# Performance work log

Measured on AMD Instinct MI355X. Metric: run time of the kernel, lower is better.

Reference implementation:

```python
import jax, jax.numpy as jnp
import numpy as np

NUM_ENT = 10000
NUM_REL = 230
S_DIM = 96
T_DIM = 32
DIM = S_DIM + T_DIM  # 128
N = 32768   # neighbors
Q = 4096    # unique query entities
E = 32768   # pooling edges
B = 1024    # batch triples
BN_EPS = 1e-5


def setup_inputs() -> dict:
    key = jax.random.key(0)
    ks = jax.random.split(key, 32)
    inp = {}
    inp["neighbor_idx"] = jax.random.randint(ks[0], (N,), 0, NUM_ENT)
    inp["rel_id"] = jax.random.randint(ks[1], (N,), 0, 2 * NUM_REL)
    inp["years"] = jax.random.uniform(ks[2], (N, 1), jnp.float32)
    inp["months"] = jax.random.uniform(ks[3], (N, 1), jnp.float32)
    inp["days"] = jax.random.uniform(ks[4], (N, 1), jnp.float32)
    inp["pool_src"] = jax.random.randint(ks[5], (E,), 0, N)
    inp["pool_dst"] = jax.random.randint(ks[6], (E,), 0, Q)
    inp["head_pos"] = jax.random.randint(ks[7], (B,), 0, Q)
    inp["tail_pos"] = jax.random.randint(ks[8], (B,), 0, Q)
    inp["rels"] = jax.random.randint(ks[9], (B,), 0, NUM_REL)
    # parameters (xavier-ish scales)
    inp["ent_embs"] = jax.random.normal(ks[10], (NUM_ENT, S_DIM), jnp.float32) * 0.05
    names = ["y_freq", "y_phi", "y_amp", "m_freq", "m_phi", "m_amp", "d_freq", "d_phi", "d_amp"]
    for i, n in enumerate(names):
        inp[n] = jax.random.normal(ks[11 + i], (NUM_ENT, T_DIM), jnp.float32) * 0.05
    inp["rel_embs"] = jax.random.normal(ks[20], (NUM_REL, DIM), jnp.float32) * 0.05
    inp["W"] = jax.random.normal(ks[21], (2 * NUM_REL, DIM, DIM), jnp.float32) * (1.0 / np.sqrt(DIM))
    inp["b"] = jnp.zeros((2 * NUM_REL, DIM), jnp.float32)
    inp["gamma"] = jnp.ones((2 * NUM_REL, DIM), jnp.float32)
    inp["beta"] = jnp.zeros((2 * NUM_REL, DIM), jnp.float32)
    return inp


def _forward(ent_embs, y_freq, y_phi, y_amp, m_freq, m_phi, m_amp,
             d_freq, d_phi, d_amp, rel_embs, W, b, gamma, beta,
             years, months, days,
             neighbor_idx, rel_id, pool_src, pool_dst, head_pos, tail_pos, rels):
    # diachronic time embedding: amp * sin(freq * t + phi), summed over y/m/d
    ty = y_amp[neighbor_idx] * jnp.sin(y_freq[neighbor_idx] * years + y_phi[neighbor_idx])
    tm = m_amp[neighbor_idx] * jnp.sin(m_freq[neighbor_idx] * months + m_phi[neighbor_idx])
    td = d_amp[neighbor_idx] * jnp.sin(d_freq[neighbor_idx] * days + d_phi[neighbor_idx])
    x = jnp.concatenate([ent_embs[neighbor_idx], ty + tm + td], axis=1)  # [N, DIM]

    # per-relation Linear (gather weights per neighbor)
    z = jnp.einsum('nd,nde->ne', x, W[rel_id]) + b[rel_id]  # [N, DIM]

    # per-relation-bucket BatchNorm (training stats, biased var); skipped for singleton buckets
    R2 = 2 * NUM_REL
    cnt = jax.ops.segment_sum(jnp.ones((z.shape[0],), z.dtype), rel_id, num_segments=R2)
    denom = jnp.maximum(cnt, 1.0)[:, None]
    mean = jax.ops.segment_sum(z, rel_id, num_segments=R2) / denom
    var = jax.ops.segment_sum(z * z, rel_id, num_segments=R2) / denom - mean * mean
    var = jnp.maximum(var, 0.0)
    zn = (z - mean[rel_id]) * jax.lax.rsqrt(var[rel_id] + BN_EPS) * gamma[rel_id] + beta[rel_id]
    z = jnp.where((cnt[rel_id] > 1.0)[:, None], zn, z)
    z = jax.nn.relu(z)

    # average pooling of neighbor features per query entity (PoolingLayer 'avg')
    psum = jax.ops.segment_sum(z[pool_src], pool_dst, num_segments=Q)
    pcnt = jax.ops.segment_sum(jnp.ones((pool_src.shape[0],), z.dtype), pool_dst, num_segments=Q)
    emb = psum / jnp.maximum(pcnt, 1.0)[:, None]  # [Q, DIM]

    # TransE-style scoring: -||h + r - t||_2 (dropout p=0 / eval mode)
    diff = emb[head_pos] + rel_embs[rels] - emb[tail_pos]
    return -jnp.sqrt(jnp.sum(diff * diff, axis=1))


def reference(neighbor_idx, rel_id, years, months, days, pool_src, pool_dst,
              head_pos, tail_pos, rels, ent_embs, y_freq, y_phi, y_amp,
              m_freq, m_phi, m_amp, d_freq, d_phi, d_amp, rel_embs, W, b, gamma, beta):
    return _forward(ent_embs, y_freq, y_phi, y_amp, m_freq, m_phi, m_amp,
                    d_freq, d_phi, d_amp, rel_embs, W, b, gamma, beta,
                    years, months, days,
                    neighbor_idx, rel_id, pool_src, pool_dst, head_pos, tail_pos, rels)
```

## Files before the change

### kernel.cpp

```cpp
#include <hip/hip_runtime.h>
#include <math.h>

#define NUM_ENT 10000
#define NUM_REL 230
#define R2      460
#define S_DIM   96
#define T_DIM   32
#define DIM     128
#define N_NBR   32768
#define Q_ENT   4096
#define E_EDGE  32768
#define B_TRI   1024
#define BN_EPS  1e-5f
#define CHUNK   64

typedef __attribute__((ext_vector_type(8))) short bf16x8;
typedef __attribute__((ext_vector_type(4))) float f32x4;

__device__ __forceinline__ unsigned short f2bf(float f) {
    unsigned int u = __float_as_uint(f);
    u = (u + 0x7FFFu + ((u >> 16) & 1u)) >> 16;
    return (unsigned short)u;
}
__device__ __forceinline__ float bf2f(unsigned short us) {
    return __uint_as_float((unsigned int)us << 16);
}

__device__ __forceinline__ int XIDX(int m, int d) {
    return (m * DIM + d) ^ ((m & 7) << 3);
}

__global__ void k_zero(int* __restrict__ p, int n4) {
    int i = blockIdx.x * blockDim.x + threadIdx.x;
    if (i < n4) ((int4*)p)[i] = make_int4(0, 0, 0, 0);
}

__global__ __launch_bounds__(256, 2) void k_front(
    const float* __restrict__ W, unsigned short* __restrict__ Wfrag,
    const int* __restrict__ rel, const int* __restrict__ psrc,
    const int* __restrict__ pdst,
    int* __restrict__ hist_rel, int* __restrict__ histE,
    int* __restrict__ hist_dst,
    int* __restrict__ ticket_n, int* __restrict__ ticket_e,
    int* __restrict__ ticket_d)
{
    const int t = threadIdx.x;
    if (blockIdx.x >= R2) {
        const int i = (blockIdx.x - R2) * 256 + t;
        if (i < N_NBR) ticket_n[i] = atomicAdd(&hist_rel[rel[i]], 1);
        if (i < E_EDGE) {
            const int s = psrc[i];
            ticket_e[i] = atomicAdd(&histE[rel[s]], 1);
            ticket_d[i] = atomicAdd(&hist_dst[pdst[i]], 1);
        }
        return;
    }
    const int r = blockIdx.x;
    __shared__ float Wl[DIM * DIM];
    {
        const float4* Wg = (const float4*)(W + (size_t)r * DIM * DIM);
        float4* Wl4 = (float4*)Wl;
        #pragma unroll
        for (int i = 0; i < 16; ++i)
            Wl4[t + i * 256] = Wg[t + i * 256];
    }
    __syncthreads();
    unsigned short* dst = Wfrag + (size_t)r * DIM * DIM;
    #pragma unroll
    for (int it = 0; it < 8; ++it) {
        const int id = t + it * 256;
        const int lane = id & 63;
        const int h    = (id >> 6) & 1;
        const int wv   = (id >> 7) & 3;
        const int kk   = (id >> 9) & 3;
        const int n  = 32 * wv + 16 * h + (lane & 15);
        const int kb = 32 * kk + 8 * (lane >> 4);
        ushort4 lo, hi;
        lo.x = f2bf(Wl[(kb + 0) * DIM + n]);
        lo.y = f2bf(Wl[(kb + 1) * DIM + n]);
        lo.z = f2bf(Wl[(kb + 2) * DIM + n]);
        lo.w = f2bf(Wl[(kb + 3) * DIM + n]);
        hi.x = f2bf(Wl[(kb + 4) * DIM + n]);
        hi.y = f2bf(Wl[(kb + 5) * DIM + n]);
        hi.z = f2bf(Wl[(kb + 6) * DIM + n]);
        hi.w = f2bf(Wl[(kb + 7) * DIM + n]);
        *(ushort4*)&dst[id * 8]     = lo;
        *(ushort4*)&dst[id * 8 + 4] = hi;
    }
}

__global__ __launch_bounds__(256) void k_place(
    const int* __restrict__ rel, const int* __restrict__ psrc,
    const int* __restrict__ pdst,
    const int* __restrict__ hist_rel, const int* __restrict__ histE,
    const int* __restrict__ hist_dst,
    const int* __restrict__ ticket_n, const int* __restrict__ ticket_e,
    const int* __restrict__ ticket_d,
    int* __restrict__ offsets, int* __restrict__ eoff, int* __restrict__ dst_off,
    int* __restrict__ order, int* __restrict__ epack)
{
    __shared__ int hA[512], hE[512], hD[4096], part[256];
    const int t = threadIdx.x;
    const int b = blockIdx.x;

    hA[t]       = (t < R2) ? hist_rel[t] : 0;
    hA[t + 256] = (t + 256 < R2) ? hist_rel[t + 256] : 0;
    hE[t]       = (t < R2) ? histE[t] : 0;
    hE[t + 256] = (t + 256 < R2) ? histE[t + 256] : 0;
    #pragma unroll
    for (int j = 0; j < 16; ++j) hD[t + j * 256] = hist_dst[t + j * 256];
    __syncthreads();

    const int a0 = hA[2 * t], a1 = hA[2 * t + 1];
    part[t] = a0 + a1;
    __syncthreads();
    for (int off = 1; off < 256; off <<= 1) {
        int v = (t >= off) ? part[t - off] : 0;
        __syncthreads();
        part[t] += v;
        __syncthreads();
    }
    {
        const int ex = t ? part[t - 1] : 0;
        hA[2 * t] = ex; hA[2 * t + 1] = ex + a0;
        if (b == 0) {
            if (2 * t < R2)     offsets[2 * t]     = ex;
            if (2 * t + 1 < R2) offsets[2 * t + 1] = ex + a0;
            if (t == 255)       offsets[R2]        = part[255];
        }
    }
    __syncthreads();

    const int b0 = hE[2 * t], b1 = hE[2 * t + 1];
    part[t] = b0 + b1;
    __syncthreads();
    for (int off = 1; off < 256; off <<= 1) {
        int v = (t >= off) ? part[t - off] : 0;
        __syncthreads();
        part[t] += v;
        __syncthreads();
    }
    {
        const int ex = t ? part[t - 1] : 0;
        hE[2 * t] = ex; hE[2 * t + 1] = ex + b0;
        if (b == 0) {
            if (2 * t < R2)     eoff[2 * t]     = ex;
            if (2 * t + 1 < R2) eoff[2 * t + 1] = ex + b0;
            if (t == 255)       eoff[R2]        = part[255];
        }
    }
    __syncthreads();

    {
        const int base = t * 16;
        int v[16]; int lsum = 0;
        #pragma unroll
        for (int j = 0; j < 16; ++j) { v[j] = hD[base + j]; lsum += v[j]; }
        part[t] = lsum;
        __syncthreads();
        for (int off = 1; off < 256; off <<= 1) {
            int vv = (t >= off) ? part[t - off] : 0;
            __syncthreads();
            part[t] += vv;
            __syncthreads();
        }
        int run = t ? part[t - 1] : 0;
        #pragma unroll
        for (int j = 0; j < 16; ++j) {
            hD[base + j] = run;
            if (b == 0) dst_off[base + j] = run;
            run += v[j];
        }
        if (b == 0 && t == 255) dst_off[4096] = run;
    }
    __syncthreads();

    const int i = b * 256 + t;
    if (i < N_NBR) {
        order[hA[rel[i]] + ticket_n[i]] = i;
    }
    if (i < E_EDGE) {
        const int s = psrc[i];
        const int row  = hA[rel[s]] + ticket_n[s];
        const int epos = hE[rel[s]] + ticket_e[i];
        const int dpos = hD[pdst[i]] + ticket_d[i];
        epack[epos] = row | (dpos << 15);
    }
}

__global__ __launch_bounds__(512, 4) void k_matvec(
    const int* __restrict__ order, const int* __restrict__ offsets,
    const int* __restrict__ eoff, const int* __restrict__ epack,
    const int* __restrict__ nbr,
    const float* __restrict__ years, const float* __restrict__ months, const float* __restrict__ days,
    const float* __restrict__ ent,
    const float* __restrict__ yf, const float* __restrict__ yp, const float* __restrict__ ya,
    const float* __restrict__ mf, const float* __restrict__ mp, const float* __restrict__ ma,
    const float* __restrict__ df, const float* __restrict__ dp, const float* __restrict__ da,
    const unsigned short* __restrict__ Wfrag, const float* __restrict__ bias,
    const float* __restrict__ gamma, const float* __restrict__ beta,
    unsigned short* __restrict__ z_s, unsigned short* __restrict__ eval)
{
    const int r     = blockIdx.x;
    const int start = offsets[r];
    const int cnt   = offsets[r + 1] - start;

    __shared__ __align__(16) unsigned short Xl[2][CHUNK * DIM];
    __shared__ int s_ord[2][CHUNK];
    __shared__ int s_ni[2][CHUNK];
    __shared__ float bnred[8][2][16][2];
    __shared__ float scl[DIM], shf[DIM];

    const int t    = threadIdx.x;
    const int wid  = t >> 6;
    const int half = wid >> 2;
    const int wv   = wid & 3;
    const int lane = t & 63;
    const int l15  = lane & 15;
    const int g    = lane >> 4;

    const int nn0 = 32 * wv + l15;
    const int nn1 = nn0 + 16;
    const float bv0 = bias[r * DIM + nn0];
    const float bv1 = bias[r * DIM + nn1];

    float lsum0 = 0.f, lsq0 = 0.f, lsum1 = 0.f, lsq1 = 0.f;
    const unsigned short* Wr = Wfrag + (size_t)r * DIM * DIM;

    for (int cbase = 0; cbase < cnt; cbase += 2 * CHUNK) {
        const int hbase = cbase + half * CHUNK;
        const int mcnt  = min(CHUNK, max(0, cnt - hbase));

        if (t < 2 * CHUNK) {
            const int hh = t >> 6;
            const int m  = t & 63;
            const int gb = cbase + hh * CHUNK;
            int o = -1, ni = 0;
            if (gb + m < cnt) { o = order[start + gb + m]; ni = nbr[o]; }
            s_ord[hh][m] = o;
            s_ni[hh][m]  = ni;
        }
        __syncthreads();

        if (mcnt > 0) {
            const int lt = t & 255;
            const int m = lt >> 2, s = lt & 3;
            const int ni = s_ni[half][m];
            const bool vm = (m < mcnt);
            #pragma unroll
            for (int kk = 0; kk < 6; ++kk) {
                const int d = 4 * (s + 4 * kk);
                float4 e = *(const float4*)(ent + (size_t)ni * S_DIM + d);
                ushort4 b;
                b.x = vm ? f2bf(e.x) : 0; b.y = vm ? f2bf(e.y) : 0;
                b.z = vm ? f2bf(e.z) : 0; b.w = vm ? f2bf(e.w) : 0;
                *(ushort4*)&Xl[half][XIDX(m, d)] = b;
            }
            const int o = s_ord[half][m] < 0 ? 0 : s_ord[half][m];
            const float yr = years[o], mo = months[o], dy = days[o];
            #pragma unroll
            for (int hh = 0; hh < 2; ++hh) {
                const int j0 = s * 8 + hh * 4;
                const size_t tb = (size_t)ni * T_DIM + j0;
                const float4 vyf = *(const float4*)(yf + tb), vyp = *(const float4*)(yp + tb), vya = *(const float4*)(ya + tb);
                const float4 vmf = *(const float4*)(mf + tb), vmp = *(const float4*)(mp + tb), vma = *(const float4*)(ma + tb);
                const float4 vdf = *(const float4*)(df + tb), vdp = *(const float4*)(dp + tb), vda = *(const float4*)(da + tb);
                ushort4 b;
                #pragma unroll
                for (int j = 0; j < 4; ++j) {
                    const float fy = ((const float*)&vyf)[j] * yr + ((const float*)&vyp)[j];
                    const float fm = ((const float*)&vmf)[j] * mo + ((const float*)&vmp)[j];
                    const float fd = ((const float*)&vdf)[j] * dy + ((const float*)&vdp)[j];
                    float v = ((const float*)&vya)[j] * sinf(fy)
                            + ((const float*)&vma)[j] * sinf(fm)
                            + ((const float*)&vda)[j] * sinf(fd);
                    ((unsigned short*)&b)[j] = vm ? f2bf(v) : 0;
                }
                *(ushort4*)&Xl[half][XIDX(m, S_DIM + j0)] = b;
            }
        }
        __syncthreads();

        if (mcnt > 0) {
            f32x4 acc[4][2];
            #pragma unroll
            for (int i = 0; i < 4; ++i)
                #pragma unroll
                for (int j = 0; j < 2; ++j) acc[i][j] = (f32x4)0.f;

            #pragma unroll
            for (int kk = 0; kk < 4; ++kk) {
                const int k0 = kk * 32;
                bf16x8 a[4];
                #pragma unroll
                for (int mt = 0; mt < 4; ++mt)
                    a[mt] = *(const bf16x8*)&Xl[half][XIDX(16 * mt + l15, k0 + 8 * g)];
                const bf16x8 b0 = *(const bf16x8*)&Wr[(size_t)((kk * 4 + wv) * 2 + 0) * 512 + lane * 8];
                const bf16x8 b1 = *(const bf16x8*)&Wr[(size_t)((kk * 4 + wv) * 2 + 1) * 512 + lane * 8];
                #pragma unroll
                for (int mt = 0; mt < 4; ++mt) {
                    acc[mt][0] = __builtin_amdgcn_mfma_f32_16x16x32_bf16(a[mt], b0, acc[mt][0], 0, 0, 0);
                    acc[mt][1] = __builtin_amdgcn_mfma_f32_16x16x32_bf16(a[mt], b1, acc[mt][1], 0, 0, 0);
                }
            }

            #pragma unroll
            for (int mt = 0; mt < 4; ++mt) {
                #pragma unroll
                for (int reg = 0; reg < 4; ++reg) {
                    const int ml = 16 * mt + 4 * g + reg;
                    if (ml < mcnt) {
                        const float v0 = acc[mt][0][reg] + bv0;
                        const float v1 = acc[mt][1][reg] + bv1;
                        const size_t row = (size_t)(start + hbase + ml) * DIM;
                        z_s[row + nn0] = f2bf(v0);
                        z_s[row + nn1] = f2bf(v1);
                        lsum0 += v0; lsq0 += v0 * v0;
                        lsum1 += v1; lsq1 += v1 * v1;
                    }
                }
            }
        }
        __syncthreads();
    }

    lsum0 += __shfl_xor(lsum0, 16); lsum0 += __shfl_xor(lsum0, 32);
    lsq0  += __shfl_xor(lsq0, 16);  lsq0  += __shfl_xor(lsq0, 32);
    lsum1 += __shfl_xor(lsum1, 16); lsum1 += __shfl_xor(lsum1, 32);
    lsq1  += __shfl_xor(lsq1, 16);  lsq1  += __shfl_xor(lsq1, 32);
    if (g == 0) {
        bnred[wid][0][l15][0] = lsum0; bnred[wid][0][l15][1] = lsq0;
        bnred[wid][1][l15][0] = lsum1; bnred[wid][1][l15][1] = lsq1;
    }
    __syncthreads();
    if (half == 0 && g == 0) {
        #pragma unroll
        for (int nt = 0; nt < 2; ++nt) {
            const int col = 32 * wv + 16 * nt + l15;
            const float s = bnred[wid][nt][l15][0] + bnred[wid + 4][nt][l15][0];
            const float q = bnred[wid][nt][l15][1] + bnred[wid + 4][nt][l15][1];
            float sc = 1.f, sh = 0.f;
            if (cnt > 1) {
                const float mean = s / (float)cnt;
                const float var  = fmaxf(q / (float)cnt - mean * mean, 0.f);
                const int gi = r * DIM + col;
                sc = gamma[gi] * rsqrtf(var + BN_EPS);
                sh = beta[gi] - mean * sc;
            }
            scl[col] = sc;
            shf[col] = sh;
        }
    }
    __syncthreads();

    {
        const int e0 = eoff[r], e1 = eoff[r + 1];
        const int grp = t >> 7;
        const int d   = t & 127;
        const float psc = scl[d], psh = shf[d];
        for (int e = e0 + grp; e < e1; e += 4) {
            const int pk   = epack[e];
            const int row  = pk & 0x7FFF;
            const int dpos = pk >> 15;
            const float v = fmaxf(bf2f(z_s[(size_t)row * DIM + d]) * psc + psh, 0.f);
            eval[(size_t)dpos * DIM + d] = f2bf(v);
        }
    }
}

__global__ void k_score(const int* __restrict__ head, const int* __restrict__ tail,
                        const int* __restrict__ rels,
                        const unsigned short* __restrict__ eval,
                        const int* __restrict__ dst_off,
                        const float* __restrict__ rel_embs,
                        float* __restrict__ out)
{
    const int b = blockIdx.x;
    const int d = threadIdx.x;
    const int h = head[b], tq = tail[b], r = rels[b];

    const int h0 = dst_off[h],  h1 = dst_off[h + 1];
    const int t0 = dst_off[tq], t1 = dst_off[tq + 1];

    float fh = 0.f;
    for (int e = h0; e < h1; ++e) fh += bf2f(eval[(size_t)e * DIM + d]);
    fh /= (float)max(h1 - h0, 1);

    float ft = 0.f;
    for (int e = t0; e < t1; ++e) ft += bf2f(eval[(size_t)e * DIM + d]);
    ft /= (float)max(t1 - t0, 1);

    const float diff = fh + rel_embs[r * DIM + d] - ft;
    float sq = diff * diff;
    for (int off = 32; off > 0; off >>= 1) sq += __shfl_down(sq, off);
    __shared__ float partial[2];
    if ((threadIdx.x & 63) == 0) partial[threadIdx.x >> 6] = sq;
    __syncthreads();
    if (threadIdx.x == 0) out[b] = -sqrtf(partial[0] + partial[1]);
}

extern "C" void kernel_launch(void* const* d_in, const int* in_sizes, int n_in,
                              void* d_out, int out_size, void* d_ws, size_t ws_size,
                              hipStream_t stream) {
    const int*   neighbor_idx = (const int*)  d_in[0];
    const int*   rel_id       = (const int*)  d_in[1];
    const float* years        = (const float*)d_in[2];
    const float* months       = (const float*)d_in[3];
    const float* days         = (const float*)d_in[4];
    const int*   pool_src     = (const int*)  d_in[5];
    const int*   pool_dst     = (const int*)  d_in[6];
    const int*   head_pos     = (const int*)  d_in[7];
    const int*   tail_pos     = (const int*)  d_in[8];
    const int*   rels         = (const int*)  d_in[9];
    const float* ent_embs     = (const float*)d_in[10];
    const float* y_freq       = (const float*)d_in[11];
    const float* y_phi        = (const float*)d_in[12];
    const float* y_amp        = (const float*)d_in[13];
    const float* m_freq       = (const float*)d_in[14];
    const float* m_phi        = (const float*)d_in[15];
    const float* m_amp        = (const float*)d_in[16];
    const float* d_freq       = (const float*)d_in[17];
    const float* d_phi        = (const float*)d_in[18];
    const float* d_amp        = (const float*)d_in[19];
    const float* rel_embs     = (const float*)d_in[20];
    const float* W            = (const float*)d_in[21];
    const float* bias         = (const float*)d_in[22];
    const float* gamma        = (const float*)d_in[23];
    const float* beta         = (const float*)d_in[24];

    float* out = (float*)d_out;

    float* ws = (float*)d_ws;
    size_t off = 0;
    unsigned short* Wfrag = (unsigned short*)(ws + off); off += (size_t)R2 * DIM * DIM / 2;
    unsigned short* z_s   = (unsigned short*)(ws + off); off += (size_t)N_NBR * DIM / 2;
    unsigned short* eval  = (unsigned short*)(ws + off); off += (size_t)E_EDGE * DIM / 2;
    int* hist_rel = (int*)(ws + off); off += R2;
    int* histE    = (int*)(ws + off); off += R2;
    int* hist_dst = (int*)(ws + off); off += Q_ENT;
    int* ticket_n = (int*)(ws + off); off += N_NBR;
    int* ticket_e = (int*)(ws + off); off += E_EDGE;
    int* ticket_d = (int*)(ws + off); off += E_EDGE;
    int* offsets  = (int*)(ws + off); off += R2 + 1;
    int* eoff     = (int*)(ws + off); off += R2 + 1;
    int* dst_off  = (int*)(ws + off); off += Q_ENT + 1;
    int* order    = (int*)(ws + off); off += N_NBR;
    int* epack    = (int*)(ws + off); off += E_EDGE;

    const int nzero  = 2 * R2 + Q_ENT;
    const int nzero4 = (nzero + 3) / 4;
    k_zero<<<(nzero4 + 255) / 256, 256, 0, stream>>>(hist_rel, nzero4);

    k_front<<<R2 + (N_NBR + 255) / 256, 256, 0, stream>>>(
        W, Wfrag, rel_id, pool_src, pool_dst,
        hist_rel, histE, hist_dst, ticket_n, ticket_e, ticket_d);

    k_place<<<(N_NBR + 255) / 256, 256, 0, stream>>>(
        rel_id, pool_src, pool_dst, hist_rel, histE, hist_dst,
        ticket_n, ticket_e, ticket_d,
        offsets, eoff, dst_off, order, epack);

    k_matvec<<<R2, 512, 0, stream>>>(order, offsets, eoff, epack,
                                     neighbor_idx,
                                     years, months, days, ent_embs,
                                     y_freq, y_phi, y_amp,
                                     m_freq, m_phi, m_amp,
                                     d_freq, d_phi, d_amp,
                                     Wfrag, bias, gamma, beta,
                                     z_s, eval);

    k_score<<<B_TRI, DIM, 0, stream>>>(head_pos, tail_pos, rels,
                                       eval, dst_off, rel_embs, out);
}
```

Baseline: 74.81 us.

## Keep pre-BN outputs in LDS and gather pooled rows via indirection in scoring

The matvec kernel now stages up to 128 pre-normalization rows per relation in shared memory and writes the normalized, ReLU'd features once per neighbor row, falling back to global memory for larger groups. It no longer scatters a copy per pooling edge. The per-edge histogram, scan and packing are removed, and the scoring kernel gathers rows through a dst-sorted row-index array instead of reading an edge-expanded buffer. This cuts global round-trips and one atomic pass. The extra 32KB of LDS may lower occupancy, and the scoring kernel now does indirect gathers with 64 threads each handling two dims.

Result: faster. 65.50 us, median of 2 (-12.5%).

```diff
diff --git a/kernel.cpp b/kernel.cpp
--- a/kernel.cpp
+++ b/kernel.cpp
@@ -13,6 +13,7 @@
 #define B_TRI   1024
 #define BN_EPS  1e-5f
 #define CHUNK   64
+#define ZCAP    128
 
 typedef __attribute__((ext_vector_type(8))) short bf16x8;
 typedef __attribute__((ext_vector_type(4))) float f32x4;
@@ -37,22 +38,15 @@
 
 __global__ __launch_bounds__(256, 2) void k_front(
     const float* __restrict__ W, unsigned short* __restrict__ Wfrag,
-    const int* __restrict__ rel, const int* __restrict__ psrc,
-    const int* __restrict__ pdst,
-    int* __restrict__ hist_rel, int* __restrict__ histE,
-    int* __restrict__ hist_dst,
-    int* __restrict__ ticket_n, int* __restrict__ ticket_e,
-    int* __restrict__ ticket_d)
+    const int* __restrict__ rel, const int* __restrict__ pdst,
+    int* __restrict__ hist_rel, int* __restrict__ hist_dst,
+    int* __restrict__ ticket_n, int* __restrict__ ticket_d)
 {
     const int t = threadIdx.x;
     if (blockIdx.x >= R2) {
         const int i = (blockIdx.x - R2) * 256 + t;
         if (i < N_NBR) ticket_n[i] = atomicAdd(&hist_rel[rel[i]], 1);
-        if (i < E_EDGE) {
-            const int s = psrc[i];
-            ticket_e[i] = atomicAdd(&histE[rel[s]], 1);
-            ticket_d[i] = atomicAdd(&hist_dst[pdst[i]], 1);
-        }
+        if (i < E_EDGE) ticket_d[i] = atomicAdd(&hist_dst[pdst[i]], 1);
         return;
     }
     const int r = blockIdx.x;
@@ -92,21 +86,17 @@
 __global__ __launch_bounds__(256) void k_place(
     const int* __restrict__ rel, const int* __restrict__ psrc,
     const int* __restrict__ pdst,
-    const int* __restrict__ hist_rel, const int* __restrict__ histE,
-    const int* __restrict__ hist_dst,
-    const int* __restrict__ ticket_n, const int* __restrict__ ticket_e,
-    const int* __restrict__ ticket_d,
-    int* __restrict__ offsets, int* __restrict__ eoff, int* __restrict__ dst_off,
-    int* __restrict__ order, int* __restrict__ epack)
+    const int* __restrict__ hist_rel, const int* __restrict__ hist_dst,
+    const int* __restrict__ ticket_n, const int* __restrict__ ticket_d,
+    int* __restrict__ offsets, int* __restrict__ dst_off,
+    int* __restrict__ order, int* __restrict__ drow)
 {
-    __shared__ int hA[512], hE[512], hD[4096], part[256];
+    __shared__ int hA[512], hD[4096], part[256];
     const int t = threadIdx.x;
     const int b = blockIdx.x;
 
     hA[t]       = (t < R2) ? hist_rel[t] : 0;
     hA[t + 256] = (t + 256 < R2) ? hist_rel[t + 256] : 0;
-    hE[t]       = (t < R2) ? histE[t] : 0;
-    hE[t + 256] = (t + 256 < R2) ? histE[t + 256] : 0;
     #pragma unroll
     for (int j = 0; j < 16; ++j) hD[t + j * 256] = hist_dst[t + j * 256];
     __syncthreads();
@@ -131,26 +121,6 @@
     }
     __syncthreads();
 
-    const int b0 = hE[2 * t], b1 = hE[2 * t + 1];
-    part[t] = b0 + b1;
-    __syncthreads();
-    for (int off = 1; off < 256; off <<= 1) {
-        int v = (t >= off) ? part[t - off] : 0;
-        __syncthreads();
-        part[t] += v;
-        __syncthreads();
-    }
-    {
-        const int ex = t ? part[t - 1] : 0;
-        hE[2 * t] = ex; hE[2 * t + 1] = ex + b0;
-        if (b == 0) {
-            if (2 * t < R2)     eoff[2 * t]     = ex;
-            if (2 * t + 1 < R2) eoff[2 * t + 1] = ex + b0;
-            if (t == 255)       eoff[R2]        = part[255];
-        }
-    }
-    __syncthreads();
-
     {
         const int base = t * 16;
         int v[16]; int lsum = 0;
@@ -182,15 +152,13 @@
     if (i < E_EDGE) {
         const int s = psrc[i];
         const int row  = hA[rel[s]] + ticket_n[s];
-        const int epos = hE[rel[s]] + ticket_e[i];
         const int dpos = hD[pdst[i]] + ticket_d[i];
-        epack[epos] = row | (dpos << 15);
+        drow[dpos] = row;
     }
 }
 
 __global__ __launch_bounds__(512, 4) void k_matvec(
     const int* __restrict__ order, const int* __restrict__ offsets,
-    const int* __restrict__ eoff, const int* __restrict__ epack,
     const int* __restrict__ nbr,
     const float* __restrict__ years, const float* __restrict__ months, const float* __restrict__ days,
     const float* __restrict__ ent,
@@ -199,13 +167,15 @@
     const float* __restrict__ df, const float* __restrict__ dp, const float* __restrict__ da,
     const unsigned short* __restrict__ Wfrag, const float* __restrict__ bias,
     const float* __restrict__ gamma, const float* __restrict__ beta,
-    unsigned short* __restrict__ z_s, unsigned short* __restrict__ eval)
+    unsigned short* __restrict__ zf)
 {
     const int r     = blockIdx.x;
     const int start = offsets[r];
     const int cnt   = offsets[r + 1] - start;
+    if (cnt == 0) return;
 
     __shared__ __align__(16) unsigned short Xl[2][CHUNK * DIM];
+    __shared__ __align__(16) unsigned short Zl[ZCAP * DIM];
     __shared__ int s_ord[2][CHUNK];
     __shared__ int s_ni[2][CHUNK];
     __shared__ float bnred[8][2][16][2];
@@ -312,9 +282,15 @@
                     if (ml < mcnt) {
                         const float v0 = acc[mt][0][reg] + bv0;
                         const float v1 = acc[mt][1][reg] + bv1;
-                        const size_t row = (size_t)(start + hbase + ml) * DIM;
-                        z_s[row + nn0] = f2bf(v0);
-                        z_s[row + nn1] = f2bf(v1);
+                        const int lrow = hbase + ml;
+                        if (lrow < ZCAP) {
+                            Zl[lrow * DIM + nn0] = f2bf(v0);
+                            Zl[lrow * DIM + nn1] = f2bf(v1);
+                        } else {
+                            const size_t row = (size_t)(start + lrow) * DIM;
+                            zf[row + nn0] = f2bf(v0);
+                            zf[row + nn1] = f2bf(v1);
+                        }
                         lsum0 += v0; lsq0 += v0 * v0;
                         lsum1 += v1; lsq1 += v1 * v1;
                     }
@@ -354,49 +330,66 @@
     __syncthreads();
 
     {
-        const int e0 = eoff[r], e1 = eoff[r + 1];
-        const int grp = t >> 7;
-        const int d   = t & 127;
-        const float psc = scl[d], psh = shf[d];
-        for (int e = e0 + grp; e < e1; e += 4) {
-            const int pk   = epack[e];
-            const int row  = pk & 0x7FFF;
-            const int dpos = pk >> 15;
-            const float v = fmaxf(bf2f(z_s[(size_t)row * DIM + d]) * psc + psh, 0.f);
-            eval[(size_t)dpos * DIM + d] = f2bf(v);
+        const int d2 = (t & 63) * 2;
+        const int grp = t >> 6;
+        const float sc0 = scl[d2],     sh0 = shf[d2];
+        const float sc1 = scl[d2 + 1], sh1 = shf[d2 + 1];
+        const int nrows = min(cnt, ZCAP);
+        for (int i = grp; i < nrows; i += 8) {
+            const ushort2 zz = *(const ushort2*)&Zl[i * DIM + d2];
+            ushort2 o;
+            o.x = f2bf(fmaxf(bf2f(zz.x) * sc0 + sh0, 0.f));
+            o.y = f2bf(fmaxf(bf2f(zz.y) * sc1 + sh1, 0.f));
+            *(ushort2*)&zf[(size_t)(start + i) * DIM + d2] = o;
+        }
+        for (int i = ZCAP + grp; i < cnt; i += 8) {
+            const size_t base = (size_t)(start + i) * DIM + d2;
+            const ushort2 zz = *(const ushort2*)&zf[base];
+            ushort2 o;
+            o.x = f2bf(fmaxf(bf2f(zz.x) * sc0 + sh0, 0.f));
+            o.y = f2bf(fmaxf(bf2f(zz.y) * sc1 + sh1, 0.f));
+            *(ushort2*)&zf[base] = o;
         }
     }
 }
 
 __global__ void k_score(const int* __restrict__ head, const int* __restrict__ tail,
                         const int* __restrict__ rels,
-                        const unsigned short* __restrict__ eval,
-                        const int* __restrict__ dst_off,
+                        const unsigned short* __restrict__ zf,
+                        const int* __restrict__ drow, const int* __restrict__ dst_off,
                         const float* __restrict__ rel_embs,
                         float* __restrict__ out)
 {
     const int b = blockIdx.x;
-    const int d = threadIdx.x;
+    const int t = threadIdx.x;
+    const int d2 = t * 2;
     const int h = head[b], tq = tail[b], r = rels[b];
 
     const int h0 = dst_off[h],  h1 = dst_off[h + 1];
     const int t0 = dst_off[tq], t1 = dst_off[tq + 1];
 
-    float fh = 0.f;
-    for (int e = h0; e < h1; ++e) fh += bf2f(eval[(size_t)e * DIM + d]);
-    fh /= (float)max(h1 - h0, 1);
-
-    float ft = 0.f;
-    for (int e = t0; e < t1; ++e) ft += bf2f(eval[(size_t)e * DIM + d]);
-    ft /= (float)max(t1 - t0, 1);
-
-    const float diff = fh + rel_embs[r * DIM + d] - ft;
-    float sq = diff * diff;
+    float fh0 = 0.f, fh1 = 0.f;
+    for (int e = h0; e < h1; ++e) {
+        const ushort2 v = *(const ushort2*)&zf[(size_t)drow[e] * DIM + d2];
+        fh0 += bf2f(v.x); fh1 += bf2f(v.y);
+    }
+    const float hn = 1.f / (float)max(h1 - h0, 1);
+    fh0 *= hn; fh1 *= hn;
+
+    float ft0 = 0.f, ft1 = 0.f;
+    for (int e = t0; e < t1; ++e) {
+        const ushort2 v = *(const ushort2*)&zf[(size_t)drow[e] * DIM + d2];
+        ft0 += bf2f(v.x); ft1 += bf2f(v.y);
+    }
+    const float tn = 1.f / (float)max(t1 - t0, 1);
+    ft0 *= tn; ft1 *= tn;
+
+    const float2 re = *(const float2*)&rel_embs[r * DIM + d2];
+    const float d0 = fh0 + re.x - ft0;
+    const float d1 = fh1 + re.y - ft1;
+    float sq = d0 * d0 + d1 * d1;
     for (int off = 32; off > 0; off >>= 1) sq += __shfl_down(sq, off);
-    __shared__ float partial[2];
-    if ((threadIdx.x & 63) == 0) partial[threadIdx.x >> 6] = sq;
-    __syncthreads();
-    if (threadIdx.x == 0) out[b] = -sqrtf(partial[0] + partial[1]);
+    if (t == 0) out[b] = -sqrtf(sq);
 }
 
 extern "C" void kernel_launch(void* const* d_in, const int* in_sizes, int n_in,
@@ -433,42 +426,37 @@
     float* ws = (float*)d_ws;
     size_t off = 0;
     unsigned short* Wfrag = (unsigned short*)(ws + off); off += (size_t)R2 * DIM * DIM / 2;
-    unsigned short* z_s   = (unsigned short*)(ws + off); off += (size_t)N_NBR * DIM / 2;
-    unsigned short* eval  = (unsigned short*)(ws + off); off += (size_t)E_EDGE * DIM / 2;
+    unsigned short* zf    = (unsigned short*)(ws + off); off += (size_t)N_NBR * DIM / 2;
     int* hist_rel = (int*)(ws + off); off += R2;
-    int* histE    = (int*)(ws + off); off += R2;
     int* hist_dst = (int*)(ws + off); off += Q_ENT;
     int* ticket_n = (int*)(ws + off); off += N_NBR;
-    int* ticket_e = (int*)(ws + off); off += E_EDGE;
     int* ticket_d = (int*)(ws + off); off += E_EDGE;
     int* offsets  = (int*)(ws + off); off += R2 + 1;
-    int* eoff     = (int*)(ws + off); off += R2 + 1;
     int* dst_off  = (int*)(ws + off); off += Q_ENT + 1;
     int* order    = (int*)(ws + off); off += N_NBR;
-    int* epack    = (int*)(ws + off); off += E_EDGE;
-
-    const int nzero  = 2 * R2 + Q_ENT;
+    int* drow     = (int*)(ws + off); off += E_EDGE;
+
+    const int nzero  = R2 + Q_ENT;
     const int nzero4 = (nzero + 3) / 4;
     k_zero<<<(nzero4 + 255) / 256, 256, 0, stream>>>(hist_rel, nzero4);
 
     k_front<<<R2 + (N_NBR + 255) / 256, 256, 0, stream>>>(
-        W, Wfrag, rel_id, pool_src, pool_dst,
-        hist_rel, histE, hist_dst, ticket_n, ticket_e, ticket_d);
+        W, Wfrag, rel_id, pool_dst,
+        hist_rel, hist_dst, ticket_n, ticket_d);
 
     k_place<<<(N_NBR + 255) / 256, 256, 0, stream>>>(
-        rel_id, pool_src, pool_dst, hist_rel, histE, hist_dst,
-        ticket_n, ticket_e, ticket_d,
-        offsets, eoff, dst_off, order, epack);
-
-    k_matvec<<<R2, 512, 0, stream>>>(order, offsets, eoff, epack,
+        rel_id, pool_src, pool_dst, hist_rel, hist_dst,
+        ticket_n, ticket_d, offsets, dst_off, order, drow);
+
+    k_matvec<<<R2, 512, 0, stream>>>(order, offsets,
                                      neighbor_idx,
                                      years, months, days, ent_embs,
                                      y_freq, y_phi, y_amp,
                                      m_freq, m_phi, m_amp,
                                      d_freq, d_phi, d_amp,
                                      Wfrag, bias, gamma, beta,
-                                     z_s, eval);
-
-    k_score<<<B_TRI, DIM, 0, stream>>>(head_pos, tail_pos, rels,
-                                       eval, dst_off, rel_embs, out);
-}
+                                     zf);
+
+    k_score<<<B_TRI, 64, 0, stream>>>(head_pos, tail_pos, rels,
+                                      zf, drow, dst_off, rel_embs, out);
+}
```
